# Performance work log

Hardware: AMD Instinct MI355X
Metric: run time of the kernel (lower is better)

Reference implementation:

```python
import math
import jax, jax.numpy as jnp
import numpy as np

B, S, D, H, HD = 2, 2048, 1024, 16, 64  # batch, seq, dim, heads, head_dim
EPS = 1e-5

def setup_inputs() -> dict:
    key = jax.random.key(0)
    ks = jax.random.split(key, 10)
    init = lambda k, shape: jax.random.normal(k, shape, jnp.float32) * 0.02
    return {
        "x": jax.random.normal(ks[0], (B, S, D), jnp.float32),
        "cos": jax.random.uniform(ks[1], (1, S, 1, 1, HD), dtype=jnp.float32),
        "sin": jax.random.uniform(ks[2], (1, S, 1, 1, HD), dtype=jnp.float32),
        "c": jax.random.normal(ks[3], (B, D), jnp.float32),
        "norm1_w": jnp.ones((D,), jnp.float32),
        "w_qkv": init(ks[4], (3 * D, D)),
        "w_out": init(ks[5], (D, D)),
        "norm2_w": jnp.ones((D,), jnp.float32),
        "mlp_w1": init(ks[6], (4 * D, D)),
        "mlp_b1": jnp.zeros((4 * D,), jnp.float32),
        "mlp_w2": init(ks[7], (D, 4 * D)),
        "mlp_b2": jnp.zeros((D,), jnp.float32),
        "ada_w": init(ks[8], (6 * D, D)),
        "ada_b": init(ks[9], (6 * D,)),
    }

def _ln(x, w):
    # LayerNorm computed in fp32, no bias, then scaled by weight
    xf = x.astype(jnp.float32)
    mu = xf.mean(-1, keepdims=True)
    var = xf.var(-1, keepdims=True)
    return (xf - mu) * jax.lax.rsqrt(var + EPS) * w

def _modulate(h, shift, scale):
    return h * (1.0 + scale[:, None, :]) + shift[:, None, :]

def reference(x, cos, sin, c, norm1_w, w_qkv, w_out, norm2_w,
              mlp_w1, mlp_b1, mlp_w2, mlp_b2, ada_w, ada_b):
    # adaLN modulation params: [B, 6D] -> six [B, D] chunks
    ada = c @ ada_w.T + ada_b
    sh_msa, sc_msa, g_msa, sh_mlp, sc_mlp, g_mlp = jnp.split(ada, 6, axis=-1)

    # attention branch (flash_attn path: no rotary applied, naive full softmax)
    h = _modulate(_ln(x, norm1_w), sh_msa, sc_msa)
    qkv = (h @ w_qkv.T).reshape(B, S, 3, H, HD)
    q, k, v = qkv[:, :, 0], qkv[:, :, 1], qkv[:, :, 2]
    scores = jnp.einsum('bqhd,bkhd->bhqk', q, k) / math.sqrt(HD)
    probs = jax.nn.softmax(scores, axis=-1)
    attn = jnp.einsum('bhqk,bkhd->bqhd', probs, v).reshape(B, S, D)
    # gate * dropout(out) + residual; eval mode -> dropout = identity
    x = x + g_msa[:, None, :] * (attn @ w_out.T)

    # MLP branch
    h = _modulate(_ln(x, norm2_w), sh_mlp, sc_mlp)
    h = jax.nn.gelu(h @ mlp_w1.T + mlp_b1, approximate=True) @ mlp_w2.T + mlp_b2
    return x + g_mlp[:, None, :] * h
```

## Files before the change

### kernel.cpp

```cpp
#include <hip/hip_runtime.h>
#include <stdint.h>

typedef __attribute__((ext_vector_type(4))) float f32x4;
typedef __attribute__((ext_vector_type(8))) __bf16 bf16x8;

#define DEV static __device__ __forceinline__

DEV unsigned short f2bf(float f){
    uint32_t u = __float_as_uint(f);
    u += 0x7FFFu + ((u >> 16) & 1u);
    return (unsigned short)(u >> 16);
}
DEV float bf2f(unsigned short s){
    uint32_t u = ((uint32_t)s) << 16;
    return __uint_as_float(u);
}

typedef __attribute__((address_space(1))) const void as1v;
typedef __attribute__((address_space(3))) void as3v;
DEV void g2l16(const void* g, void* l){
    __builtin_amdgcn_global_load_lds((as1v*)g, (as3v*)l, 16, 0, 0);
}

__global__ __launch_bounds__(256) void k_cast_bf16(const float* __restrict__ in,
                                                   unsigned short* __restrict__ out, int n4){
    int i = blockIdx.x * 256 + threadIdx.x;
    if (i < n4){
        float4 v = ((const float4*)in)[i];
        ((ushort4*)out)[i] = make_ushort4(f2bf(v.x), f2bf(v.y), f2bf(v.z), f2bf(v.w));
    }
}

__global__ __launch_bounds__(256) void k_ada(const float* __restrict__ c,
                                             const float* __restrict__ aw,
                                             const float* __restrict__ ab,
                                             float* __restrict__ out){
    int wid  = blockIdx.x * 4 + (threadIdx.x >> 6);
    int lane = threadIdx.x & 63;
    int b = wid / 6144, r = wid % 6144;
    const float4* cw = (const float4*)(c + (size_t)b * 1024);
    const float4* wr = (const float4*)(aw + (size_t)r * 1024);
    float s = 0.f;
    #pragma unroll
    for (int i = 0; i < 4; i++){
        float4 a = wr[lane + i * 64];
        float4 q = cw[lane + i * 64];
        s += a.x*q.x + a.y*q.y + a.z*q.z + a.w*q.w;
    }
    #pragma unroll
    for (int off = 32; off > 0; off >>= 1) s += __shfl_down(s, off);
    if (lane == 0) out[wid] = s + ab[r];
}

__global__ __launch_bounds__(256) void k_ln_mod(const float* __restrict__ x,
                                                const float* __restrict__ w,
                                                const float* __restrict__ ada,
                                                int sh_off, int sc_off,
                                                unsigned short* __restrict__ out){
    int row = blockIdx.x;
    int b   = row >> 11;
    int tid = threadIdx.x;
    float4 v = ((const float4*)(x + (size_t)row * 1024))[tid];
    float s  = v.x + v.y + v.z + v.w;
    float ss = v.x*v.x + v.y*v.y + v.z*v.z + v.w*v.w;
    #pragma unroll
    for (int off = 32; off > 0; off >>= 1){ s += __shfl_down(s, off); ss += __shfl_down(ss, off); }
    __shared__ float red[8];
    int wv = tid >> 6;
    if ((tid & 63) == 0){ red[wv] = s; red[4 + wv] = ss; }
    __syncthreads();
    float S  = red[0] + red[1] + red[2] + red[3];
    float SS = red[4] + red[5] + red[6] + red[7];
    float mu   = S * (1.f / 1024.f);
    float rstd = rsqrtf(SS * (1.f / 1024.f) - mu * mu + 1e-5f);
    const float* adab = ada + (size_t)b * 6144;
    float4 wv4 = ((const float4*)w)[tid];
    float4 sh  = ((const float4*)(adab + sh_off))[tid];
    float4 sc  = ((const float4*)(adab + sc_off))[tid];
    float h0 = (v.x - mu) * rstd * wv4.x * (1.f + sc.x) + sh.x;
    float h1 = (v.y - mu) * rstd * wv4.y * (1.f + sc.y) + sh.y;
    float h2 = (v.z - mu) * rstd * wv4.z * (1.f + sc.z) + sh.z;
    float h3 = (v.w - mu) * rstd * wv4.w * (1.f + sc.w) + sh.w;
    ((ushort4*)(out + (size_t)row * 1024))[tid] = make_ushort4(f2bf(h0), f2bf(h1), f2bf(h2), f2bf(h3));
}

template<int MODE>
__global__ __launch_bounds__(256) void k_gemm(const unsigned short* __restrict__ A,
                                              const unsigned short* __restrict__ B,
                                              void* __restrict__ outp,
                                              const float* __restrict__ bias,
                                              const float* __restrict__ res,
                                              const float* __restrict__ ada, int goff,
                                              int M, int N, int K){
    __shared__ unsigned short As[3 * 4096];
    __shared__ unsigned short Bs[3 * 4096];
    int tid = threadIdx.x, lane = tid & 63, wv = tid >> 6;
    int quad = lane >> 4, l15 = lane & 15;
    int wm = wv & 1, wn = wv >> 1;
    int bm = blockIdx.x, bn = blockIdx.y;
    int klo, khi;
    if constexpr (MODE == 3){
        klo = blockIdx.z * 1376;
        khi = klo + 1376; if (khi > K) khi = K;
    } else {
        int kpb = K / gridDim.z;
        klo = blockIdx.z * kpb; khi = klo + kpb;
    }
    f32x4 acc[4][4] = {};
    int srow = wv * 16 + (lane >> 2), sseg = lane & 3;
    const unsigned short* ga = A + (size_t)(bm * 128 + srow) * K + sseg * 8;
    const unsigned short* gb = B + (size_t)(bn * 128 + srow) * K + sseg * 8;
    size_t stride64 = (size_t)64 * K;
    int wb = wv * 512;
    int nt = (khi - klo) >> 5;
    auto STAGE = [&](int t, int bufi){
        unsigned short* as = As + bufi * 4096;
        unsigned short* bs = Bs + bufi * 4096;
        int ko = klo + (t << 5);
        g2l16(ga + ko,            as + wb);
        g2l16(ga + stride64 + ko, as + 2048 + wb);
        g2l16(gb + ko,            bs + wb);
        g2l16(gb + stride64 + ko, bs + 2048 + wb);
    };
    STAGE(0, 0);
    STAGE(1, 1);
    for (int t = 0; t < nt; ++t){
        int bi = t % 3;
        if (t){
            __builtin_amdgcn_s_barrier();
            __builtin_amdgcn_sched_barrier(0);
        }
        if (t + 2 < nt) STAGE(t + 2, (t + 2) % 3);
        if (t + 2 < nt)      asm volatile("s_waitcnt vmcnt(8)" ::: "memory");
        else if (t + 1 < nt) asm volatile("s_waitcnt vmcnt(4)" ::: "memory");
        else                 asm volatile("s_waitcnt vmcnt(0)" ::: "memory");
        __builtin_amdgcn_s_barrier();
        __builtin_amdgcn_sched_barrier(0);
        const unsigned short* as = As + bi * 4096;
        const unsigned short* bs = Bs + bi * 4096;
        bf16x8 af[4], bfr[4];
        #pragma unroll
        for (int i = 0; i < 4; i++)
            af[i] = *(const bf16x8*)(as + (wm * 64 + i * 16 + l15) * 32 + quad * 8);
        #pragma unroll
        for (int j = 0; j < 4; j++)
            bfr[j] = *(const bf16x8*)(bs + (wn * 64 + j * 16 + l15) * 32 + quad * 8);
        #pragma unroll
        for (int i = 0; i < 4; i++)
            #pragma unroll
            for (int j = 0; j < 4; j++)
                acc[i][j] = __builtin_amdgcn_mfma_f32_16x16x32_bf16(af[i], bfr[j], acc[i][j], 0, 0, 0);
    }
    unsigned short* zp = nullptr;
    if constexpr (MODE == 3){
        int z = blockIdx.z;
        if (z < 2) zp = (unsigned short*)outp + (size_t)z * 4194304;
        else       zp = (unsigned short*)(void*)bias;
    }
    int row0 = bm * 128 + wm * 64, col0 = bn * 128 + wn * 64;
    #pragma unroll
    for (int i = 0; i < 4; i++){
        #pragma unroll
        for (int r = 0; r < 4; r++){
            int row = row0 + i * 16 + quad * 4 + r;
            #pragma unroll
            for (int j = 0; j < 4; j++){
                int col = col0 + j * 16 + l15;
                float v = acc[i][j][r];
                size_t idx = (size_t)row * N + col;
                if constexpr (MODE == 0){
                    ((unsigned short*)outp)[idx] = f2bf(v);
                } else if constexpr (MODE == 1){
                    float t = v + bias[col];
                    float u = 1.5957691216057308f * (t + 0.044715f * t * t * t);
                    float g = t / (1.f + __expf(-u));
                    ((unsigned short*)outp)[idx] = f2bf(g);
                } else if constexpr (MODE == 2){
                    float t = v;
                    if (bias) t += bias[col];
                    int bb = row >> 11;
                    float g = ada[(size_t)bb * 6144 + goff + col];
                    ((float*)outp)[idx] = res[idx] + g * t;
                } else {
                    zp[idx] = f2bf(v);
                }
            }
        }
    }
}

__global__ __launch_bounds__(256) void k_ep2(const unsigned short* __restrict__ z01,
                                             const unsigned short* __restrict__ z2,
                                             const float* __restrict__ bias,
                                             const float* __restrict__ res,
                                             const float* __restrict__ ada, int goff,
                                             float* __restrict__ out){
    int row = blockIdx.x;
    int bb  = row >> 11;
    int tid = threadIdx.x;
    size_t base = (size_t)row * 1024 + tid * 4;
    ushort4 a0 = *(const ushort4*)(z01 + base);
    ushort4 a1 = *(const ushort4*)(z01 + 4194304 + base);
    ushort4 a2 = *(const ushort4*)(z2 + base);
    float4 rv = *(const float4*)(res + base);
    float4 bv = ((const float4*)bias)[tid];
    float4 gv = ((const float4*)(ada + (size_t)bb * 6144 + goff))[tid];
    float4 o;
    o.x = rv.x + gv.x * (bf2f(a0.x) + bf2f(a1.x) + bf2f(a2.x) + bv.x);
    o.y = rv.y + gv.y * (bf2f(a0.y) + bf2f(a1.y) + bf2f(a2.y) + bv.y);
    o.z = rv.z + gv.z * (bf2f(a0.z) + bf2f(a1.z) + bf2f(a2.z) + bv.z);
    o.w = rv.w + gv.w * (bf2f(a0.w) + bf2f(a1.w) + bf2f(a2.w) + bv.w);
    *(float4*)(out + base) = o;
}

__global__ __launch_bounds__(256) void k_vt(const unsigned short* __restrict__ qkv,
                                            unsigned short* __restrict__ vt){
    __shared__ unsigned short T[64 * 66];
    int kb = blockIdx.x, bh = blockIdx.y;
    int b = bh >> 4, h = bh & 15;
    size_t rb = (size_t)b * 2048;
    int t = threadIdx.x;
    int key = t >> 2, seg = t & 3;
    const unsigned short* src = qkv + (rb + kb * 64 + key) * 3072 + 2048 + h * 64;
    uint4 v0 = *(const uint4*)(src + seg * 8);
    uint4 v1 = *(const uint4*)(src + 32 + seg * 8);
    const unsigned short* p0 = (const unsigned short*)&v0;
    const unsigned short* p1 = (const unsigned short*)&v1;
    unsigned short* tr = T + key * 66;
    ushort2* t0 = (ushort2*)(tr + seg * 8);
    ushort2* t1 = (ushort2*)(tr + 32 + seg * 8);
    #pragma unroll
    for (int j = 0; j < 4; j++){
        t0[j] = make_ushort2(p0[2*j], p0[2*j+1]);
        t1[j] = make_ushort2(p1[2*j], p1[2*j+1]);
    }
    __syncthreads();
    int d = t >> 2, kseg = t & 3;
    unsigned short obuf[16];
    #pragma unroll
    for (int j = 0; j < 16; j++) obuf[j] = T[(kseg * 16 + j) * 66 + d];
    uint4* dst = (uint4*)(vt + ((size_t)bh * 64 + d) * 2048 + kb * 64 + kseg * 16);
    dst[0] = ((const uint4*)obuf)[0];
    dst[1] = ((const uint4*)obuf)[1];
}

__global__ __launch_bounds__(256) void k_attn(const unsigned short* __restrict__ qkv,
                                              const unsigned short* __restrict__ vt,
                                              unsigned short* __restrict__ out){
    __shared__ unsigned short Ks[2 * 4096];
    __shared__ unsigned short Vs[2 * 4096];
    __shared__ __align__(16) unsigned short Ps[4 * 32 * 72];
    int tid = threadIdx.x, lane = tid & 63, wv = tid >> 6;
    int quad = lane >> 4, l15 = lane & 15;
    int qt = blockIdx.x, bh = blockIdx.y;
    int b = bh >> 4, h = bh & 15;
    size_t rb = (size_t)b * 2048;

    bf16x8 qb[2][2];
    #pragma unroll
    for (int t = 0; t < 2; t++){
        int qrow = qt * 128 + wv * 32 + t * 16 + l15;
        const unsigned short* qp = qkv + ((rb + qrow) * 3072 + h * 64 + quad * 8);
        qb[t][0] = *(const bf16x8*)qp;
        qb[t][1] = *(const bf16x8*)(qp + 32);
    }
    float lsum[2] = {0.f, 0.f};
    f32x4 o[2][4];
    #pragma unroll
    for (int t = 0; t < 2; t++)
        #pragma unroll
        for (int dt = 0; dt < 4; dt++) o[t][dt] = (f32x4){0.f, 0.f, 0.f, 0.f};

    int rr = wv * 16 + (lane >> 2), cs = lane & 3;
    const unsigned short* gk = qkv + (rb + rr) * 3072 + 1024 + h * 64 + cs * 8;
    const unsigned short* gv = vt + ((size_t)bh * 64 + rr) * 2048 + cs * 8;
    int soff = rr * 32 + (cs ^ ((rr >> 1) & 3)) * 8;
    int rsl = (quad ^ ((l15 >> 1) & 3)) * 8;
    unsigned short* Pw = Ps + wv * 32 * 72;

    uint4 rk0 = *(const uint4*)(gk);
    uint4 rk1 = *(const uint4*)(gk + 32);
    uint4 rv0 = *(const uint4*)(gv);
    uint4 rv1 = *(const uint4*)(gv + 32);

    for (int k0 = 0; k0 < 2048; k0 += 64){
        unsigned short* ks = Ks + ((k0 >> 6) & 1) * 4096;
        unsigned short* vs = Vs + ((k0 >> 6) & 1) * 4096;
        int kn = (k0 + 64 < 2048) ? (k0 + 64) : k0;
        uint4 nk0 = *(const uint4*)(gk + (size_t)kn * 3072);
        uint4 nk1 = *(const uint4*)(gk + (size_t)kn * 3072 + 32);
        uint4 nv0 = *(const uint4*)(gv + kn);
        uint4 nv1 = *(const uint4*)(gv + kn + 32);
        *(uint4*)(ks + soff)        = rk0;
        *(uint4*)(ks + 2048 + soff) = rk1;
        *(uint4*)(vs + soff)        = rv0;
        *(uint4*)(vs + 2048 + soff) = rv1;
        __syncthreads();
        rk0 = nk0; rk1 = nk1; rv0 = nv0; rv1 = nv1;
        f32x4 c[2][4];
        #pragma unroll
        for (int kt = 0; kt < 4; kt++){
            bf16x8 ka0 = *(const bf16x8*)(ks + (kt * 16 + l15) * 32 + rsl);
            bf16x8 ka1 = *(const bf16x8*)(ks + 2048 + (kt * 16 + l15) * 32 + rsl);
            #pragma unroll
            for (int t = 0; t < 2; t++){
                f32x4 z = (f32x4){0.f, 0.f, 0.f, 0.f};
                z = __builtin_amdgcn_mfma_f32_16x16x32_bf16(ka0, qb[t][0], z, 0, 0, 0);
                z = __builtin_amdgcn_mfma_f32_16x16x32_bf16(ka1, qb[t][1], z, 0, 0, 0);
                c[t][kt] = z;
            }
        }
        #pragma unroll
        for (int t = 0; t < 2; t++){
            #pragma unroll
            for (int kt = 0; kt < 4; kt++){
                float p0 = __expf(c[t][kt][0] * 0.125f);
                float p1 = __expf(c[t][kt][1] * 0.125f);
                float p2 = __expf(c[t][kt][2] * 0.125f);
                float p3 = __expf(c[t][kt][3] * 0.125f);
                lsum[t] += (p0 + p1) + (p2 + p3);
                union { uint2 u; __bf16 bh4[4]; } w;
                w.bh4[0] = (__bf16)p0;
                w.bh4[1] = (__bf16)p1;
                w.bh4[2] = (__bf16)p2;
                w.bh4[3] = (__bf16)p3;
                *(uint2*)(Pw + (t * 16 + l15) * 72 + kt * 16 + quad * 4) = w.u;
            }
        }
        bf16x8 pa[2][2];
        #pragma unroll
        for (int t = 0; t < 2; t++){
            pa[t][0] = *(const bf16x8*)(Pw + (t * 16 + l15) * 72 + quad * 8);
            pa[t][1] = *(const bf16x8*)(Pw + (t * 16 + l15) * 72 + 32 + quad * 8);
        }
        #pragma unroll
        for (int dt = 0; dt < 4; dt++){
            bf16x8 vb0 = *(const bf16x8*)(vs + (dt * 16 + l15) * 32 + rsl);
            bf16x8 vb1 = *(const bf16x8*)(vs + 2048 + (dt * 16 + l15) * 32 + rsl);
            #pragma unroll
            for (int t = 0; t < 2; t++){
                o[t][dt] = __builtin_amdgcn_mfma_f32_16x16x32_bf16(pa[t][0], vb0, o[t][dt], 0, 0, 0);
                o[t][dt] = __builtin_amdgcn_mfma_f32_16x16x32_bf16(pa[t][1], vb1, o[t][dt], 0, 0, 0);
            }
        }
    }
    #pragma unroll
    for (int t = 0; t < 2; t++){
        lsum[t] += __shfl_xor(lsum[t], 16);
        lsum[t] += __shfl_xor(lsum[t], 32);
    }
    #pragma unroll
    for (int t = 0; t < 2; t++){
        #pragma unroll
        for (int r = 0; r < 4; r++){
            float lt = __shfl(lsum[t], quad * 4 + r);
            float inv = 1.f / lt;
            int row = qt * 128 + wv * 32 + t * 16 + quad * 4 + r;
            unsigned short* op = out + ((rb + row) * 1024 + h * 64);
            #pragma unroll
            for (int dt = 0; dt < 4; dt++)
                op[dt * 16 + l15] = f2bf(o[t][dt][r] * inv);
        }
    }
}

extern "C" void kernel_launch(void* const* d_in, const int* in_sizes, int n_in,
                              void* d_out, int out_size, void* d_ws, size_t ws_size,
                              hipStream_t stream){
    const float* x     = (const float*)d_in[0];
    const float* c     = (const float*)d_in[3];
    const float* n1w   = (const float*)d_in[4];
    const float* w_qkv = (const float*)d_in[5];
    const float* w_out = (const float*)d_in[6];
    const float* n2w   = (const float*)d_in[7];
    const float* w1    = (const float*)d_in[8];
    const float* b1    = (const float*)d_in[9];
    const float* w2    = (const float*)d_in[10];
    const float* b2    = (const float*)d_in[11];
    const float* ada_w = (const float*)d_in[12];
    const float* ada_b = (const float*)d_in[13];
    float* out = (float*)d_out;
    char* ws = (char*)d_ws;

    unsigned short* wqkv_b = (unsigned short*)(ws + 0);
    unsigned short* wout_b = (unsigned short*)(ws + 6291456);
    unsigned short* w1_b   = (unsigned short*)(ws + 8388608);
    unsigned short* w2_b   = (unsigned short*)(ws + 16777216);
    float*          ada    = (float*)         (ws + 25165824);
    unsigned short* h      = (unsigned short*)(ws + 25214976);
    unsigned short* qkv    = (unsigned short*)(ws + 33603584);
    unsigned short* attn   = (unsigned short*)(ws + 58769408);
    float*          xn     = (float*)         (ws + 67158016);
    unsigned short* u      = qkv;
    unsigned short* vt     = h;
    unsigned short* z01 = (unsigned short*)(ws + 0);
    unsigned short* z2  = (unsigned short*)(ws + 25214976);

    k_cast_bf16<<<3072, 256, 0, stream>>>(w_qkv, wqkv_b,  786432);
    k_cast_bf16<<<1024, 256, 0, stream>>>(w_out, wout_b,  262144);
    k_cast_bf16<<<4096, 256, 0, stream>>>(w1,    w1_b,   1048576);
    k_cast_bf16<<<4096, 256, 0, stream>>>(w2,    w2_b,   1048576);
    k_ada<<<3072, 256, 0, stream>>>(c, ada_w, ada_b, ada);
    k_ln_mod<<<4096, 256, 0, stream>>>(x, n1w, ada, 0, 1024, h);
    k_gemm<0><<<dim3(32, 24), 256, 0, stream>>>(h, wqkv_b, qkv, nullptr, nullptr, nullptr, 0, 4096, 3072, 1024);
    k_vt<<<dim3(32, 32), 256, 0, stream>>>(qkv, vt);
    k_attn<<<dim3(16, 32), 256, 0, stream>>>(qkv, vt, attn);
    k_gemm<2><<<dim3(32, 8), 256, 0, stream>>>(attn, wout_b, xn, nullptr, x, ada, 2048, 4096, 1024, 1024);
    k_ln_mod<<<4096, 256, 0, stream>>>(xn, n2w, ada, 3072, 4096, h);
    k_gemm<1><<<dim3(32, 32), 256, 0, stream>>>(h, w1_b, u, b1, nullptr, nullptr, 0, 4096, 4096, 1024);
    k_gemm<3><<<dim3(32, 8, 3), 256, 0, stream>>>(u, w2_b, z01, (const float*)z2, nullptr,
                                                  nullptr, 0, 4096, 1024, 4096);
    k_ep2<<<4096, 256, 0, stream>>>(z01, z2, b2, xn, ada, 5120, out);
}
```

Measured before the change: 395.0 us.

## Add 256x128-tile double-buffered GEMM for QKV and MLP projections

```diff
diff --git a/kernel.cpp b/kernel.cpp
--- a/kernel.cpp
+++ b/kernel.cpp
@@ -85,6 +85,93 @@
 }
 
 template<int MODE>
+__global__ __launch_bounds__(256, 2) void k_gemm2(const unsigned short* __restrict__ A,
+                                                  const unsigned short* __restrict__ B,
+                                                  void* __restrict__ outp,
+                                                  const float* __restrict__ bias,
+                                                  const float* __restrict__ res,
+                                                  const float* __restrict__ ada, int goff,
+                                                  int M, int N, int K){
+    __shared__ unsigned short S[2 * 12288];
+    int tid = threadIdx.x, lane = tid & 63, wv = tid >> 6;
+    int quad = lane >> 4, l15 = lane & 15;
+    int wm = wv & 1, wn = wv >> 1;
+    int bm = blockIdx.x, bn = blockIdx.y;
+    int klo, khi;
+    if constexpr (MODE == 3){
+        klo = blockIdx.z * 1376;
+        khi = klo + 1376; if (khi > K) khi = K;
+    } else {
+        klo = 0; khi = K;
+    }
+    f32x4 acc[8][4] = {};
+    int srow = lane >> 2, sseg = lane & 3;
+    const unsigned short* ga = A + (size_t)(bm * 256 + wv * 64 + srow) * K + sseg * 8;
+    const unsigned short* gb = B + (size_t)(bn * 128 + wv * 32 + srow) * K + sseg * 8;
+    size_t k16 = (size_t)16 * K;
+    auto STAGE = [&](int buf, int k0){
+        unsigned short* as = S + buf * 12288 + wv * 2048;
+        unsigned short* bs = S + buf * 12288 + 8192 + wv * 1024;
+        g2l16(ga + k0,            as);
+        g2l16(ga + k16 + k0,      as + 512);
+        g2l16(ga + 2 * k16 + k0,  as + 1024);
+        g2l16(ga + 3 * k16 + k0,  as + 1536);
+        g2l16(gb + k0,            bs);
+        g2l16(gb + k16 + k0,      bs + 512);
+    };
+    STAGE(0, klo);
+    for (int k0 = klo; k0 < khi; k0 += 32){
+        int cur = ((k0 - klo) >> 5) & 1;
+        __syncthreads();
+        if (k0 + 32 < khi) STAGE(cur ^ 1, k0 + 32);
+        const unsigned short* as = S + cur * 12288;
+        const unsigned short* bs = S + cur * 12288 + 8192;
+        bf16x8 af[8], bf[4];
+        #pragma unroll
+        for (int i = 0; i < 8; i++)
+            af[i] = *(const bf16x8*)(as + (wm * 128 + i * 16 + l15) * 32 + quad * 8);
+        #pragma unroll
+        for (int j = 0; j < 4; j++)
+            bf[j] = *(const bf16x8*)(bs + (wn * 64 + j * 16 + l15) * 32 + quad * 8);
+        #pragma unroll
+        for (int i = 0; i < 8; i++)
+            #pragma unroll
+            for (int j = 0; j < 4; j++)
+                acc[i][j] = __builtin_amdgcn_mfma_f32_16x16x32_bf16(af[i], bf[j], acc[i][j], 0, 0, 0);
+    }
+    unsigned short* zp = nullptr;
+    if constexpr (MODE == 3){
+        int z = blockIdx.z;
+        if (z < 2) zp = (unsigned short*)outp + (size_t)z * 4194304;
+        else       zp = (unsigned short*)(void*)bias;
+    }
+    int row0 = bm * 256 + wm * 128, col0 = bn * 128 + wn * 64;
+    #pragma unroll
+    for (int i = 0; i < 8; i++){
+        #pragma unroll
+        for (int r = 0; r < 4; r++){
+            int row = row0 + i * 16 + quad * 4 + r;
+            #pragma unroll
+            for (int j = 0; j < 4; j++){
+                int col = col0 + j * 16 + l15;
+                float v = acc[i][j][r];
+                size_t idx = (size_t)row * N + col;
+                if constexpr (MODE == 0){
+                    ((unsigned short*)outp)[idx] = f2bf(v);
+                } else if constexpr (MODE == 1){
+                    float t = v + bias[col];
+                    float u = 1.5957691216057308f * (t + 0.044715f * t * t * t);
+                    float g = t / (1.f + __expf(-u));
+                    ((unsigned short*)outp)[idx] = f2bf(g);
+                } else {
+                    zp[idx] = f2bf(v);
+                }
+            }
+        }
+    }
+}
+
+template<int MODE>
 __global__ __launch_bounds__(256) void k_gemm(const unsigned short* __restrict__ A,
                                               const unsigned short* __restrict__ B,
                                               void* __restrict__ outp,
@@ -98,14 +185,7 @@
     int quad = lane >> 4, l15 = lane & 15;
     int wm = wv & 1, wn = wv >> 1;
     int bm = blockIdx.x, bn = blockIdx.y;
-    int klo, khi;
-    if constexpr (MODE == 3){
-        klo = blockIdx.z * 1376;
-        khi = klo + 1376; if (khi > K) khi = K;
-    } else {
-        int kpb = K / gridDim.z;
-        klo = blockIdx.z * kpb; khi = klo + kpb;
-    }
+    int klo = 0, khi = K;
     f32x4 acc[4][4] = {};
     int srow = wv * 16 + (lane >> 2), sseg = lane & 3;
     const unsigned short* ga = A + (size_t)(bm * 128 + srow) * K + sseg * 8;
@@ -151,12 +231,6 @@
             for (int j = 0; j < 4; j++)
                 acc[i][j] = __builtin_amdgcn_mfma_f32_16x16x32_bf16(af[i], bfr[j], acc[i][j], 0, 0, 0);
     }
-    unsigned short* zp = nullptr;
-    if constexpr (MODE == 3){
-        int z = blockIdx.z;
-        if (z < 2) zp = (unsigned short*)outp + (size_t)z * 4194304;
-        else       zp = (unsigned short*)(void*)bias;
-    }
     int row0 = bm * 128 + wm * 64, col0 = bn * 128 + wn * 64;
     #pragma unroll
     for (int i = 0; i < 4; i++){
@@ -168,21 +242,14 @@
                 int col = col0 + j * 16 + l15;
                 float v = acc[i][j][r];
                 size_t idx = (size_t)row * N + col;
-                if constexpr (MODE == 0){
-                    ((unsigned short*)outp)[idx] = f2bf(v);
-                } else if constexpr (MODE == 1){
-                    float t = v + bias[col];
-                    float u = 1.5957691216057308f * (t + 0.044715f * t * t * t);
-                    float g = t / (1.f + __expf(-u));
-                    ((unsigned short*)outp)[idx] = f2bf(g);
-                } else if constexpr (MODE == 2){
-                    float t = v;
-                    if (bias) t += bias[col];
+                if constexpr (MODE == 2){
+                    float t2 = v;
+                    if (bias) t2 += bias[col];
                     int bb = row >> 11;
                     float g = ada[(size_t)bb * 6144 + goff + col];
-                    ((float*)outp)[idx] = res[idx] + g * t;
+                    ((float*)outp)[idx] = res[idx] + g * t2;
                 } else {
-                    zp[idx] = f2bf(v);
+                    ((unsigned short*)outp)[idx] = f2bf(v);
                 }
             }
         }
@@ -402,13 +469,13 @@
     k_cast_bf16<<<4096, 256, 0, stream>>>(w2,    w2_b,   1048576);
     k_ada<<<3072, 256, 0, stream>>>(c, ada_w, ada_b, ada);
     k_ln_mod<<<4096, 256, 0, stream>>>(x, n1w, ada, 0, 1024, h);
-    k_gemm<0><<<dim3(32, 24), 256, 0, stream>>>(h, wqkv_b, qkv, nullptr, nullptr, nullptr, 0, 4096, 3072, 1024);
+    k_gemm2<0><<<dim3(16, 24), 256, 0, stream>>>(h, wqkv_b, qkv, nullptr, nullptr, nullptr, 0, 4096, 3072, 1024);
     k_vt<<<dim3(32, 32), 256, 0, stream>>>(qkv, vt);
     k_attn<<<dim3(16, 32), 256, 0, stream>>>(qkv, vt, attn);
     k_gemm<2><<<dim3(32, 8), 256, 0, stream>>>(attn, wout_b, xn, nullptr, x, ada, 2048, 4096, 1024, 1024);
     k_ln_mod<<<4096, 256, 0, stream>>>(xn, n2w, ada, 3072, 4096, h);
-    k_gemm<1><<<dim3(32, 32), 256, 0, stream>>>(h, w1_b, u, b1, nullptr, nullptr, 0, 4096, 4096, 1024);
-    k_gemm<3><<<dim3(32, 8, 3), 256, 0, stream>>>(u, w2_b, z01, (const float*)z2, nullptr,
-                                                  nullptr, 0, 4096, 1024, 4096);
+    k_gemm2<1><<<dim3(16, 32), 256, 0, stream>>>(h, w1_b, u, b1, nullptr, nullptr, 0, 4096, 4096, 1024);
+    k_gemm2<3><<<dim3(16, 8, 3), 256, 0, stream>>>(u, w2_b, z01, (const float*)z2, nullptr,
+                                                   nullptr, 0, 4096, 1024, 4096);
     k_ep2<<<4096, 256, 0, stream>>>(z01, z2, b2, xn, ada, 5120, out);
 }
```

Measured after the change: 384.3 us. 1.03x faster.
